# Optimization experiments

Hardware: AMD Instinct MI355X
Metric: run time of the kernel (lower is better)

The kernel has to match this reference:

```python
import jax, jax.numpy as jnp
import numpy as np

N_EVENTS = 4_000_000
T_WINDOW = 100.0


def setup_inputs() -> dict:
    key = jax.random.key(0)
    k_ts, = jax.random.split(key, 1)
    # sorted event times in [0, T)
    ts = jnp.sort(jax.random.uniform(k_ts, (N_EVENTS,), dtype=jnp.float32) * T_WINDOW)
    mu = jnp.float32(0.5)
    log_alpha = jnp.log(jnp.float32(0.5))   # alpha = 0.5 (branching ratio < 1)
    log_beta = jnp.log(jnp.float32(2.0))    # beta = 2.0
    return {"ts": ts, "mu": mu, "log_alpha": log_alpha, "log_beta": log_beta, "T": 100}


def reference(ts, mu, log_alpha, log_beta, T):
    """Log-likelihood of a univariate exponential-kernel Hawkes process.

    Equivalent to UnivariateHawkesProcess.likelihood(ts, T, log=True,
    num_integration_points=0, analy_kernel=True), but the O(N^2) per-event
    Python loop is replaced by a stable O(N) exclusive cumulative logsumexp:
        sum_{j<i} exp(-beta (t_i - t_j)) = exp(logcumsumexp(beta t)_{i-1} - beta t_i)
    """
    alpha = jnp.exp(log_alpha)
    beta = jnp.exp(log_beta)
    Tf = jnp.asarray(T, dtype=ts.dtype)

    b_ts = beta * ts                               # [N]
    incl = jax.lax.cumlogsumexp(b_ts)              # inclusive running logsumexp
    excl = jnp.concatenate([jnp.full((1,), -jnp.inf, dtype=b_ts.dtype), incl[:-1]])
    decay_sum = jnp.exp(excl - b_ts)               # sum_{j<i} exp(-beta(t_i - t_j))
    intensities = mu + alpha * beta * decay_sum    # lambda(t_i | history)
    positive_ll = jnp.sum(jnp.log(intensities))

    # analytic compensator: mu*T + sum_i alpha/beta * (1 - exp(-beta (T - t_i)))
    integral = mu * Tf + jnp.sum((alpha / beta) * (1.0 - jnp.exp(-beta * (Tf - ts))))
    return positive_ll - integral
```

## Files before the change

kernel.cpp:

```cpp
#include <hip/hip_runtime.h>

#define SEG 16
#define TPB 256

struct DA { float d, a; };

__device__ __forceinline__ DA da_compose(DA f, DA g) {
    DA r; r.d = f.d * g.d; r.a = fmaf(f.a, g.d, g.a); return r;
}

__global__ void __launch_bounds__(TPB) hawkes_k1(
    const float* __restrict__ ts, const float* __restrict__ lb_p,
    const int* __restrict__ T_p, int N, int NSEG,
    DA* __restrict__ blkDA, double* __restrict__ acc, unsigned* __restrict__ ticket)
{
    const float beta = __expf(*lb_p);
    const float Tf = (float)(*T_p);
    const int tid = threadIdx.x;
    const int g = blockIdx.x * TPB + tid;
    const int lane = tid & 63, wave = tid >> 6;

    if (blockIdx.x == 0 && tid == 0) { *acc = 0.0; *ticket = 0u; }

    DA my; my.d = 1.f; my.a = 0.f;
    if (g < NSEG) {
        const int start = g * SEG;
        const int end = min(start + SEG, N);
        float R = 1.f, t0, tlast;
        if (end == start + SEG) {
            const float4* p = (const float4*)(ts + start);
            float4 a = p[0], b = p[1], c = p[2], d = p[3];
            t0 = a.x;
            float tp = a.x;
#define K1S(tt) { R = fmaf(R, __expf(-beta * ((tt) - tp)), 1.f); tp = (tt); }
            K1S(a.y) K1S(a.z) K1S(a.w)
            K1S(b.x) K1S(b.y) K1S(b.z) K1S(b.w)
            K1S(c.x) K1S(c.y) K1S(c.z) K1S(c.w)
            K1S(d.x) K1S(d.y) K1S(d.z) K1S(d.w)
#undef K1S
            tlast = d.w;
        } else {
            t0 = ts[start]; tlast = t0;
            for (int j = start + 1; j < end; ++j) {
                float t = ts[j];
                R = fmaf(R, __expf(-beta * (t - tlast)), 1.f); tlast = t;
            }
        }
        const float rnext = (end < N) ? ts[end] : Tf;
        my.a = R * __expf(-beta * (rnext - tlast));
        my.d = __expf(-beta * (rnext - t0));
    }

    DA inc = my;
    #pragma unroll
    for (int off = 1; off < 64; off <<= 1) {
        DA up; up.d = __shfl_up(inc.d, off); up.a = __shfl_up(inc.a, off);
        if (lane >= off) inc = da_compose(up, inc);
    }
    __shared__ DA wagg[TPB / 64];
    if (lane == 63) wagg[wave] = inc;
    __syncthreads();
    if (tid == 0) {
        DA aggr = wagg[0];
        #pragma unroll
        for (int w = 1; w < TPB / 64; ++w) aggr = da_compose(aggr, wagg[w]);
        blkDA[blockIdx.x] = aggr;
    }
}

__global__ void __launch_bounds__(TPB) hawkes_k2(
    const float* __restrict__ ts,
    const float* __restrict__ mu_p, const float* __restrict__ la_p,
    const float* __restrict__ lb_p, const int* __restrict__ T_p,
    int N, int NSEG, int NB,
    const DA* __restrict__ blkDA, double* __restrict__ acc,
    unsigned* __restrict__ ticket, float* __restrict__ out)
{
    const float beta  = __expf(*lb_p);
    const float mu    = *mu_p;
    const float alpha = __expf(*la_p);
    const float ab    = alpha * beta;
    const float Tf    = (float)(*T_p);
    const int tid = threadIdx.x;
    const int g = blockIdx.x * TPB + tid;
    const int lane = tid & 63, wave = tid >> 6;

    float e[SEG];
    DA my; my.d = 1.f; my.a = 0.f;
    bool full = false;
    const int start = g * SEG;
    const int end = (g < NSEG) ? min(start + SEG, N) : start;
    if (g < NSEG) {
        full = (end == start + SEG);
        float R = 1.f, t0, tlast;
        if (full) {
            const float4* p = (const float4*)(ts + start);
            float4 a = p[0], b = p[1], c = p[2], d = p[3];
            t0 = a.x;
            e[1]  = __expf(-beta * (a.y - a.x));
            e[2]  = __expf(-beta * (a.z - a.y));
            e[3]  = __expf(-beta * (a.w - a.z));
            e[4]  = __expf(-beta * (b.x - a.w));
            e[5]  = __expf(-beta * (b.y - b.x));
            e[6]  = __expf(-beta * (b.z - b.y));
            e[7]  = __expf(-beta * (b.w - b.z));
            e[8]  = __expf(-beta * (c.x - b.w));
            e[9]  = __expf(-beta * (c.y - c.x));
            e[10] = __expf(-beta * (c.z - c.y));
            e[11] = __expf(-beta * (c.w - c.z));
            e[12] = __expf(-beta * (d.x - c.w));
            e[13] = __expf(-beta * (d.y - d.x));
            e[14] = __expf(-beta * (d.z - d.y));
            e[15] = __expf(-beta * (d.w - d.z));
            #pragma unroll
            for (int k = 1; k < SEG; ++k) R = fmaf(R, e[k], 1.f);
            tlast = d.w;
        } else {
            t0 = ts[start]; tlast = t0;
            for (int j = start + 1; j < end; ++j) {
                float t = ts[j];
                R = fmaf(R, __expf(-beta * (t - tlast)), 1.f); tlast = t;
            }
        }
        const float rnext = (end < N) ? ts[end] : Tf;
        my.a = R * __expf(-beta * (rnext - tlast));
        my.d = __expf(-beta * (rnext - t0));
    }

    DA inc = my;
    #pragma unroll
    for (int off = 1; off < 64; off <<= 1) {
        DA up; up.d = __shfl_up(inc.d, off); up.a = __shfl_up(inc.a, off);
        if (lane >= off) inc = da_compose(up, inc);
    }
    __shared__ DA wagg[TPB / 64];
    if (lane == 63) wagg[wave] = inc;
    __syncthreads();
    DA pre; pre.d = 1.f; pre.a = 0.f;
    for (int w = 0; w < wave; ++w) pre = da_compose(pre, wagg[w]);
    DA lexcl; lexcl.d = __shfl_up(inc.d, 1); lexcl.a = __shfl_up(inc.a, 1);
    if (lane == 0) { lexcl.d = 1.f; lexcl.a = 0.f; }
    DA excl = da_compose(pre, lexcl);

    const int CH = (NB + TPB - 1) / TPB;
    DA comp; comp.d = 1.f; comp.a = 0.f;
    for (int j = 0; j < CH; ++j) {
        const int idx = tid * CH + j;
        if (idx < NB) comp = da_compose(comp, blkDA[idx]);
    }
    DA inc2 = comp;
    #pragma unroll
    for (int off = 1; off < 64; off <<= 1) {
        DA up; up.d = __shfl_up(inc2.d, off); up.a = __shfl_up(inc2.a, off);
        if (lane >= off) inc2 = da_compose(up, inc2);
    }
    __shared__ DA wagg2[TPB / 64];
    if (lane == 63) wagg2[wave] = inc2;
    __syncthreads();
    DA pre2; pre2.d = 1.f; pre2.a = 0.f;
    for (int w = 0; w < wave; ++w) pre2 = da_compose(pre2, wagg2[w]);
    DA lex2; lex2.d = __shfl_up(inc2.d, 1); lex2.a = __shfl_up(inc2.a, 1);
    if (lane == 0) { lex2.d = 1.f; lex2.a = 0.f; }
    DA chunkExcl = da_compose(pre2, lex2);

    __shared__ DA exclArr[TPB];
    __shared__ DA totalSh;
    exclArr[tid] = chunkExcl;
    if (tid == TPB - 1) totalSh = da_compose(pre2, inc2);
    __syncthreads();

    const int b = blockIdx.x;
    const int c0 = b / CH, pp = b - c0 * CH;
    DA E = exclArr[c0];
    for (int j = 0; j < pp; ++j) E = da_compose(E, blkDA[c0 * CH + j]);
    const float carry = E.a;
    const float S_T = totalSh.a;

    float S = fmaf(carry, excl.d, excl.a);
    float lsum = 0.f;
    if (g < NSEG) {
        if (full) {
            lsum += __logf(fmaf(ab, S, mu));
            #pragma unroll
            for (int k = 1; k < SEG; ++k) {
                float ek = e[k];
                S = fmaf(S, ek, ek);
                lsum += __logf(fmaf(ab, S, mu));
            }
        } else {
            float tprev = ts[start];
            lsum += __logf(fmaf(ab, S, mu));
            for (int j = start + 1; j < end; ++j) {
                float t = ts[j];
                float ee = __expf(-beta * (t - tprev));
                S = fmaf(S, ee, ee);
                lsum += __logf(fmaf(ab, S, mu));
                tprev = t;
            }
        }
    }

    #pragma unroll
    for (int off = 32; off > 0; off >>= 1) lsum += __shfl_down(lsum, off);
    __shared__ float wsum[TPB / 64];
    if (lane == 0) wsum[wave] = lsum;
    __syncthreads();
    if (tid == 0) {
        float tot = 0.f;
        #pragma unroll
        for (int w = 0; w < TPB / 64; ++w) tot += wsum[w];
        atomicAdd(acc, (double)tot);
        __threadfence();
        unsigned old = atomicAdd(ticket, 1u);
        if (old == (unsigned)(NB - 1)) {
            __threadfence();
            double tt = atomicAdd(acc, 0.0);
            const float integral = mu * Tf + (alpha / beta) * ((float)N - S_T);
            out[0] = (float)(tt - (double)integral);
        }
    }
}

extern "C" void kernel_launch(void* const* d_in, const int* in_sizes, int n_in,
                              void* d_out, int out_size, void* d_ws, size_t ws_size,
                              hipStream_t stream) {
    const float* ts = (const float*)d_in[0];
    const float* mu = (const float*)d_in[1];
    const float* la = (const float*)d_in[2];
    const float* lb = (const float*)d_in[3];
    const int*   T  = (const int*)d_in[4];
    const int N = in_sizes[0];
    const int NSEG = (N + SEG - 1) / SEG;
    const int NB = (NSEG + TPB - 1) / TPB;

    char* w = (char*)d_ws;
    double*   acc    = (double*)w;
    unsigned* ticket = (unsigned*)(w + 8);
    DA*       blkDA  = (DA*)(w + 16);

    hawkes_k1<<<NB, TPB, 0, stream>>>(ts, lb, T, N, NSEG, blkDA, acc, ticket);
    hawkes_k2<<<NB, TPB, 0, stream>>>(ts, mu, la, lb, T, N, NSEG, NB, blkDA, acc, ticket,
                                      (float*)d_out);
}
```

Before: 100.1 us.

## Replace two-pass scan with single-pass decoupled look-back prefix scan

Merges the reduce kernel and the scan kernel into one kernel. Blocks publish their aggregates and inclusive prefixes through 64-bit atomics, and wave 0 of each block walks backwards over predecessors to build its carry. This removes the second read of the timestamps and one kernel launch, and the integral term now folds into the last block's contribution. In exchange it adds two memset launches, spin-waiting on predecessor blocks, and a reliance on blocks being scheduled in roughly increasing order to avoid stalls.

After: 101.9 us. Within noise of the previous version (+1.8%).

```diff
diff --git a/kernel.cpp b/kernel.cpp
--- a/kernel.cpp
+++ b/kernel.cpp
@@ -3,86 +3,38 @@
 #define SEG 16
 #define TPB 256
 
+typedef unsigned long long u64;
+#define INVALID64 0xAAAAAAAAAAAAAAAAULL
+
 struct DA { float d, a; };
 
 __device__ __forceinline__ DA da_compose(DA f, DA g) {
     DA r; r.d = f.d * g.d; r.a = fmaf(f.a, g.d, g.a); return r;
 }
-
-__global__ void __launch_bounds__(TPB) hawkes_k1(
-    const float* __restrict__ ts, const float* __restrict__ lb_p,
-    const int* __restrict__ T_p, int N, int NSEG,
-    DA* __restrict__ blkDA, double* __restrict__ acc, unsigned* __restrict__ ticket)
-{
-    const float beta = __expf(*lb_p);
-    const float Tf = (float)(*T_p);
-    const int tid = threadIdx.x;
-    const int g = blockIdx.x * TPB + tid;
-    const int lane = tid & 63, wave = tid >> 6;
-
-    if (blockIdx.x == 0 && tid == 0) { *acc = 0.0; *ticket = 0u; }
-
-    DA my; my.d = 1.f; my.a = 0.f;
-    if (g < NSEG) {
-        const int start = g * SEG;
-        const int end = min(start + SEG, N);
-        float R = 1.f, t0, tlast;
-        if (end == start + SEG) {
-            const float4* p = (const float4*)(ts + start);
-            float4 a = p[0], b = p[1], c = p[2], d = p[3];
-            t0 = a.x;
-            float tp = a.x;
-#define K1S(tt) { R = fmaf(R, __expf(-beta * ((tt) - tp)), 1.f); tp = (tt); }
-            K1S(a.y) K1S(a.z) K1S(a.w)
-            K1S(b.x) K1S(b.y) K1S(b.z) K1S(b.w)
-            K1S(c.x) K1S(c.y) K1S(c.z) K1S(c.w)
-            K1S(d.x) K1S(d.y) K1S(d.z) K1S(d.w)
-#undef K1S
-            tlast = d.w;
-        } else {
-            t0 = ts[start]; tlast = t0;
-            for (int j = start + 1; j < end; ++j) {
-                float t = ts[j];
-                R = fmaf(R, __expf(-beta * (t - tlast)), 1.f); tlast = t;
-            }
-        }
-        const float rnext = (end < N) ? ts[end] : Tf;
-        my.a = R * __expf(-beta * (rnext - tlast));
-        my.d = __expf(-beta * (rnext - t0));
-    }
-
-    DA inc = my;
-    #pragma unroll
-    for (int off = 1; off < 64; off <<= 1) {
-        DA up; up.d = __shfl_up(inc.d, off); up.a = __shfl_up(inc.a, off);
-        if (lane >= off) inc = da_compose(up, inc);
-    }
-    __shared__ DA wagg[TPB / 64];
-    if (lane == 63) wagg[wave] = inc;
-    __syncthreads();
-    if (tid == 0) {
-        DA aggr = wagg[0];
-        #pragma unroll
-        for (int w = 1; w < TPB / 64; ++w) aggr = da_compose(aggr, wagg[w]);
-        blkDA[blockIdx.x] = aggr;
-    }
-}
-
-__global__ void __launch_bounds__(TPB) hawkes_k2(
+__device__ __forceinline__ u64 da_pack(DA x) {
+    return ((u64)__float_as_uint(x.a) << 32) | (u64)__float_as_uint(x.d);
+}
+__device__ __forceinline__ DA da_unpack(u64 v) {
+    DA x; x.d = __uint_as_float((unsigned)v); x.a = __uint_as_float((unsigned)(v >> 32)); return x;
+}
+
+__global__ void __launch_bounds__(TPB) hawkes_sp(
     const float* __restrict__ ts,
     const float* __restrict__ mu_p, const float* __restrict__ la_p,
     const float* __restrict__ lb_p, const int* __restrict__ T_p,
     int N, int NSEG, int NB,
-    const DA* __restrict__ blkDA, double* __restrict__ acc,
-    unsigned* __restrict__ ticket, float* __restrict__ out)
+    u64* __restrict__ aggs, u64* __restrict__ prefs,
+    double* __restrict__ acc, unsigned* __restrict__ ticket,
+    float* __restrict__ out)
 {
     const float beta  = __expf(*lb_p);
     const float mu    = *mu_p;
     const float alpha = __expf(*la_p);
     const float ab    = alpha * beta;
     const float Tf    = (float)(*T_p);
-    const int tid = threadIdx.x;
-    const int g = blockIdx.x * TPB + tid;
+    const int tid  = threadIdx.x;
+    const int b    = blockIdx.x;
+    const int g    = b * TPB + tid;
     const int lane = tid & 63, wave = tid >> 6;
 
     float e[SEG];
@@ -95,36 +47,43 @@
         float R = 1.f, t0, tlast;
         if (full) {
             const float4* p = (const float4*)(ts + start);
-            float4 a = p[0], b = p[1], c = p[2], d = p[3];
+            float4 a = p[0], bb = p[1], c = p[2], d = p[3];
             t0 = a.x;
-            e[1]  = __expf(-beta * (a.y - a.x));
-            e[2]  = __expf(-beta * (a.z - a.y));
-            e[3]  = __expf(-beta * (a.w - a.z));
-            e[4]  = __expf(-beta * (b.x - a.w));
-            e[5]  = __expf(-beta * (b.y - b.x));
-            e[6]  = __expf(-beta * (b.z - b.y));
-            e[7]  = __expf(-beta * (b.w - b.z));
-            e[8]  = __expf(-beta * (c.x - b.w));
-            e[9]  = __expf(-beta * (c.y - c.x));
-            e[10] = __expf(-beta * (c.z - c.y));
-            e[11] = __expf(-beta * (c.w - c.z));
-            e[12] = __expf(-beta * (d.x - c.w));
-            e[13] = __expf(-beta * (d.y - d.x));
-            e[14] = __expf(-beta * (d.z - d.y));
-            e[15] = __expf(-beta * (d.w - d.z));
+            e[1]  = __expf(-beta * (a.y  - a.x));
+            e[2]  = __expf(-beta * (a.z  - a.y));
+            e[3]  = __expf(-beta * (a.w  - a.z));
+            e[4]  = __expf(-beta * (bb.x - a.w));
+            e[5]  = __expf(-beta * (bb.y - bb.x));
+            e[6]  = __expf(-beta * (bb.z - bb.y));
+            e[7]  = __expf(-beta * (bb.w - bb.z));
+            e[8]  = __expf(-beta * (c.x  - bb.w));
+            e[9]  = __expf(-beta * (c.y  - c.x));
+            e[10] = __expf(-beta * (c.z  - c.y));
+            e[11] = __expf(-beta * (c.w  - c.z));
+            e[12] = __expf(-beta * (d.x  - c.w));
+            e[13] = __expf(-beta * (d.y  - d.x));
+            e[14] = __expf(-beta * (d.z  - d.y));
+            e[15] = __expf(-beta * (d.w  - d.z));
             #pragma unroll
             for (int k = 1; k < SEG; ++k) R = fmaf(R, e[k], 1.f);
             tlast = d.w;
+            float tnext = __shfl_down(t0, 1);
+            if (lane == 63 || g + 1 >= NSEG) tnext = (end < N) ? ts[end] : Tf;
+            my.a = R * __expf(-beta * (tnext - tlast));
+            my.d = __expf(-beta * (tnext - t0));
         } else {
             t0 = ts[start]; tlast = t0;
             for (int j = start + 1; j < end; ++j) {
                 float t = ts[j];
                 R = fmaf(R, __expf(-beta * (t - tlast)), 1.f); tlast = t;
             }
-        }
-        const float rnext = (end < N) ? ts[end] : Tf;
-        my.a = R * __expf(-beta * (rnext - tlast));
-        my.d = __expf(-beta * (rnext - t0));
+            __shfl_down(t0, 1);
+            const float tnext = (end < N) ? ts[end] : Tf;
+            my.a = R * __expf(-beta * (tnext - tlast));
+            my.d = __expf(-beta * (tnext - t0));
+        }
+    } else {
+        __shfl_down(0.f, 1);
     }
 
     DA inc = my;
@@ -142,41 +101,57 @@
     if (lane == 0) { lexcl.d = 1.f; lexcl.a = 0.f; }
     DA excl = da_compose(pre, lexcl);
 
-    const int CH = (NB + TPB - 1) / TPB;
-    DA comp; comp.d = 1.f; comp.a = 0.f;
-    for (int j = 0; j < CH; ++j) {
-        const int idx = tid * CH + j;
-        if (idx < NB) comp = da_compose(comp, blkDA[idx]);
-    }
-    DA inc2 = comp;
-    #pragma unroll
-    for (int off = 1; off < 64; off <<= 1) {
-        DA up; up.d = __shfl_up(inc2.d, off); up.a = __shfl_up(inc2.a, off);
-        if (lane >= off) inc2 = da_compose(up, inc2);
-    }
-    __shared__ DA wagg2[TPB / 64];
-    if (lane == 63) wagg2[wave] = inc2;
-    __syncthreads();
-    DA pre2; pre2.d = 1.f; pre2.a = 0.f;
-    for (int w = 0; w < wave; ++w) pre2 = da_compose(pre2, wagg2[w]);
-    DA lex2; lex2.d = __shfl_up(inc2.d, 1); lex2.a = __shfl_up(inc2.a, 1);
-    if (lane == 0) { lex2.d = 1.f; lex2.a = 0.f; }
-    DA chunkExcl = da_compose(pre2, lex2);
-
-    __shared__ DA exclArr[TPB];
-    __shared__ DA totalSh;
-    exclArr[tid] = chunkExcl;
-    if (tid == TPB - 1) totalSh = da_compose(pre2, inc2);
-    __syncthreads();
-
-    const int b = blockIdx.x;
-    const int c0 = b / CH, pp = b - c0 * CH;
-    DA E = exclArr[c0];
-    for (int j = 0; j < pp; ++j) E = da_compose(E, blkDA[c0 * CH + j]);
-    const float carry = E.a;
-    const float S_T = totalSh.a;
-
-    float S = fmaf(carry, excl.d, excl.a);
+    __shared__ DA blockAggSh;
+    __shared__ float carrySh, stSh;
+    if (tid == TPB - 1) {
+        DA agg = da_compose(pre, inc);
+        blockAggSh = agg;
+        atomicExch(&aggs[b], da_pack(agg));
+    }
+    __syncthreads();
+
+    if (wave == 0) {
+        DA carry; carry.d = 1.f; carry.a = 0.f;
+        int pos = b;
+        while (pos > 0) {
+            const int w = min(64, pos);
+            const int idx = pos - w + lane;
+            u64 av = INVALID64, pv = INVALID64;
+            if (lane < w) {
+                do { av = atomicAdd(&aggs[idx], 0ULL); } while (av == INVALID64);
+                pv = atomicAdd(&prefs[idx], 0ULL);
+            }
+            const u64 pmask = __ballot(pv != INVALID64);
+            DA val; val.d = 1.f; val.a = 0.f;
+            if (lane < w) val = da_unpack(av);
+            int h = -1;
+            if (pmask) h = 63 - __clzll(pmask);
+            if (h >= 0) {
+                if (lane < h) { val.d = 1.f; val.a = 0.f; }
+                else if (lane == h) val = da_unpack(pv);
+            }
+            DA winc = val;
+            #pragma unroll
+            for (int off = 1; off < 64; off <<= 1) {
+                DA up; up.d = __shfl_up(winc.d, off); up.a = __shfl_up(winc.a, off);
+                if (lane >= off) winc = da_compose(up, winc);
+            }
+            DA W; W.d = __shfl(winc.d, 63); W.a = __shfl(winc.a, 63);
+            carry = da_compose(W, carry);
+            if (h >= 0) break;
+            pos -= w;
+        }
+        DA I = da_compose(carry, blockAggSh);
+        if (lane == 0) {
+            atomicExch(&prefs[b], da_pack(I));
+            carrySh = carry.a;
+            stSh = I.a;
+        }
+    }
+    __syncthreads();
+
+    const float bc = carrySh;
+    float S = fmaf(bc, excl.d, excl.a);
     float lsum = 0.f;
     if (g < NSEG) {
         if (full) {
@@ -209,14 +184,18 @@
         float tot = 0.f;
         #pragma unroll
         for (int w = 0; w < TPB / 64; ++w) tot += wsum[w];
-        atomicAdd(acc, (double)tot);
+        double add = (double)tot;
+        if (b == NB - 1) {
+            const float integral = mu * Tf + (alpha / beta) * ((float)N - stSh);
+            add -= (double)integral;
+        }
+        atomicAdd(acc, add);
         __threadfence();
         unsigned old = atomicAdd(ticket, 1u);
         if (old == (unsigned)(NB - 1)) {
             __threadfence();
             double tt = atomicAdd(acc, 0.0);
-            const float integral = mu * Tf + (alpha / beta) * ((float)N - S_T);
-            out[0] = (float)(tt - (double)integral);
+            out[0] = (float)tt;
         }
     }
 }
@@ -236,9 +215,11 @@
     char* w = (char*)d_ws;
     double*   acc    = (double*)w;
     unsigned* ticket = (unsigned*)(w + 8);
-    DA*       blkDA  = (DA*)(w + 16);
-
-    hawkes_k1<<<NB, TPB, 0, stream>>>(ts, lb, T, N, NSEG, blkDA, acc, ticket);
-    hawkes_k2<<<NB, TPB, 0, stream>>>(ts, mu, la, lb, T, N, NSEG, NB, blkDA, acc, ticket,
-                                      (float*)d_out);
-}
+    u64*      aggs   = (u64*)(w + 16);
+    u64*      prefs  = (u64*)(w + 16 + (size_t)NB * 8);
+
+    hipMemsetAsync(w, 0, 16, stream);
+    hipMemsetAsync((void*)aggs, 0xAA, (size_t)NB * 16, stream);
+    hawkes_sp<<<NB, TPB, 0, stream>>>(ts, mu, la, lb, T, N, NSEG, NB,
+                                      aggs, prefs, acc, ticket, (float*)d_out);
+}
```
